# Kernel tuning notes

Measured on AMD Instinct MI355X. Metric: run time of the kernel, lower is better.

The kernel has to match this reference:

```python
import jax, jax.numpy as jnp
import numpy as np

LN_EPS = 1e-12  # config.layer_norm_eps (BERT default)


def setup_inputs() -> dict:
    key = jax.random.key(0)
    k1, k2, k3, k4 = jax.random.split(key, 4)
    B, S, D_IN, D_OUT = 16, 512, 4096, 1024
    return {
        "hidden_states": jax.random.normal(k1, (B, S, D_IN), dtype=jnp.float32),
        "input_tensor": jax.random.normal(k2, (B, S, D_OUT), dtype=jnp.float32),
        "W": jax.random.normal(k3, (D_OUT, D_IN), dtype=jnp.float32) * 0.02,
        "b": jax.random.normal(k4, (D_OUT,), dtype=jnp.float32) * 0.02,
        "gamma": jnp.ones((D_OUT,), dtype=jnp.float32),
        "beta": jnp.zeros((D_OUT,), dtype=jnp.float32),
    }


def reference(hidden_states, input_tensor, W, b, gamma, beta):
    # mix_Linear 1-bit path (XNOR-Net style): binarize weights with per-row scale
    alpha = jnp.mean(jnp.abs(W), axis=1, keepdims=True)   # [D_OUT, 1]
    W_q = jnp.sign(W) * alpha                              # [D_OUT, D_IN]
    # dense GEMM: [B,S,D_IN] x [D_OUT,D_IN]^T -> [B,S,D_OUT]
    h = jnp.einsum("bsi,oi->bso", hidden_states, W_q) + b
    # dropout is identity in eval mode; residual add + LayerNorm
    x = h + input_tensor
    mu = jnp.mean(x, axis=-1, keepdims=True)
    var = jnp.mean(jnp.square(x - mu), axis=-1, keepdims=True)
    return gamma * (x - mu) * jax.lax.rsqrt(var + LN_EPS) + beta
```

## Files before the change

kernel.cpp:

```cpp
#include <hip/hip_runtime.h>
#include <hip/hip_bf16.h>

using u16    = unsigned short;
using short8 = __attribute__((ext_vector_type(8))) short;
using u16x4  = __attribute__((ext_vector_type(4))) u16;
using f32x4  = __attribute__((ext_vector_type(4))) float;

#define M_DIM 8192
#define N_DIM 1024
#define K_DIM 4096

typedef __attribute__((address_space(1))) void gvoid;
typedef __attribute__((address_space(3))) void svoid;
#define GLOAD_LDS16(g, s) \
  __builtin_amdgcn_global_load_lds((gvoid*)(void*)(g), (svoid*)(s), 16, 0, 0)

__global__ __launch_bounds__(256) void wprep_kernel(const float* __restrict__ W,
                                                    u16* __restrict__ Wsgn,
                                                    float* __restrict__ alpha) {
  const int row = blockIdx.x;
  const int t   = threadIdx.x;
  const float4* wr = (const float4*)(W + (size_t)row * K_DIM);
  float4 v[4];
  float s = 0.f;
#pragma unroll
  for (int j = 0; j < 4; ++j) {
    v[j] = wr[t + 256 * j];
    s += fabsf(v[j].x) + fabsf(v[j].y) + fabsf(v[j].z) + fabsf(v[j].w);
  }
#pragma unroll
  for (int off = 32; off > 0; off >>= 1) s += __shfl_down(s, off, 64);
  __shared__ float red[4];
  if ((t & 63) == 0) red[t >> 6] = s;
  __syncthreads();
  if (t == 0) alpha[row] = (red[0] + red[1] + red[2] + red[3]) * (1.0f / K_DIM);
  u16x4* dst = (u16x4*)(Wsgn + (size_t)row * K_DIM);
#pragma unroll
  for (int j = 0; j < 4; ++j) {
    u16x4 sg;
    sg[0] = v[j].x > 0.f ? 0x3F80 : (v[j].x < 0.f ? 0xBF80 : 0);
    sg[1] = v[j].y > 0.f ? 0x3F80 : (v[j].y < 0.f ? 0xBF80 : 0);
    sg[2] = v[j].z > 0.f ? 0x3F80 : (v[j].z < 0.f ? 0xBF80 : 0);
    sg[3] = v[j].w > 0.f ? 0x3F80 : (v[j].w < 0.f ? 0xBF80 : 0);
    dst[t + 256 * j] = sg;
  }
}

__device__ __forceinline__ short8 pack_bf16x8(f32x4 lo, f32x4 hi) {
  union { short8 s; __hip_bfloat162 h[4]; } u;
  u.h[0] = __float22bfloat162_rn(make_float2(lo[0], lo[1]));
  u.h[1] = __float22bfloat162_rn(make_float2(lo[2], lo[3]));
  u.h[2] = __float22bfloat162_rn(make_float2(hi[0], hi[1]));
  u.h[3] = __float22bfloat162_rn(make_float2(hi[2], hi[3]));
  return u.s;
}

__global__ __launch_bounds__(256) void gemm_kernel(const float* __restrict__ A,
                                                   const u16* __restrict__ Bsgn,
                                                   const float* __restrict__ alpha,
                                                   const float* __restrict__ bias,
                                                   const float* __restrict__ resid,
                                                   float* __restrict__ out) {
  __shared__ float lA[2][128 * 32];
  __shared__ u16   lB[128 * 64];
  const int tid  = threadIdx.x;
  const int wave = tid >> 6;
  const int lane = tid & 63;
  const int quad = lane >> 4;
  const int l16  = lane & 15;
  const int wm   = (wave >> 1) * 64;
  const int wn   = (wave & 1) * 64;

  const int b    = blockIdx.x;
  const int xcd  = b & 7;
  const int l    = b >> 3;
  const size_t m0 = (size_t)(xcd * 8 + (l >> 3)) * 128;
  const size_t n0 = (size_t)(l & 7) * 128;

  f32x4 acc[4][4] = {};

  const int r8 = lane >> 3;
  const int s_ = lane & 7;

  const u16*   bsrc[4];
  u16*         bdst[4];
  const float* a0src[4];
  const float* a1src[4];
  float*       a0dst[4];
  float*       a1dst[4];
#pragma unroll
  for (int j = 0; j < 4; ++j) {
    const int c   = wave * 4 + j;
    const int row = c * 8 + r8;
    bsrc[j]  = Bsgn + (n0 + (size_t)row) * K_DIM + (size_t)((s_ ^ r8) * 8);
    bdst[j]  = lB + c * 512;
    a0src[j] = A + (m0 + (size_t)row) * K_DIM + (size_t)((s_ ^ r8) * 8);
    a1src[j] = a0src[j] + 4;
    a0dst[j] = &lA[0][c * 256 + lane * 4];
    a1dst[j] = &lA[1][c * 256 + lane * 4];
  }

  for (int k0 = 0; k0 < K_DIM; k0 += 64) {
#pragma unroll
    for (int j = 0; j < 4; ++j) GLOAD_LDS16(bsrc[j] + k0, bdst[j]);
#pragma unroll
    for (int j = 0; j < 4; ++j) GLOAD_LDS16(a0src[j] + k0, a0dst[j]);
#pragma unroll
    for (int j = 0; j < 4; ++j) GLOAD_LDS16(a1src[j] + k0, a1dst[j]);
    asm volatile("s_waitcnt vmcnt(0)" ::: "memory");
    __syncthreads();

#pragma unroll
    for (int s = 0; s < 2; ++s) {
      const int kq = s * 4 + quad;
      short8 af[4], bf[4];
#pragma unroll
      for (int mt = 0; mt < 4; ++mt) {
        const int row  = wm + mt * 16 + l16;
        const int slot = kq ^ (row & 7);
        f32x4 lo = *(const f32x4*)(&lA[0][row * 32 + slot * 4]);
        f32x4 hi = *(const f32x4*)(&lA[1][row * 32 + slot * 4]);
        af[mt] = pack_bf16x8(lo, hi);
      }
#pragma unroll
      for (int nt = 0; nt < 4; ++nt) {
        const int col = wn + nt * 16 + l16;
        bf[nt] = *(const short8*)(lB + col * 64 + ((kq ^ (col & 7)) * 8));
      }
#pragma unroll
      for (int mt = 0; mt < 4; ++mt)
#pragma unroll
        for (int nt = 0; nt < 4; ++nt)
          acc[mt][nt] = __builtin_amdgcn_mfma_f32_16x16x32_bf16(af[mt], bf[nt],
                                                                acc[mt][nt], 0, 0, 0);
    }
    __syncthreads();
  }

#pragma unroll
  for (int nt = 0; nt < 4; ++nt) {
    const size_t n  = n0 + wn + nt * 16 + l16;
    const float  al = alpha[n];
    const float  bi = bias[n];
#pragma unroll
    for (int mt = 0; mt < 4; ++mt) {
      const size_t mbase = m0 + wm + mt * 16 + quad * 4;
#pragma unroll
      for (int r = 0; r < 4; ++r) {
        const size_t mm = mbase + r;
        out[mm * N_DIM + n] = acc[mt][nt][r] * al + bi + resid[mm * N_DIM + n];
      }
    }
  }
}

__global__ __launch_bounds__(256) void ln_kernel(float* __restrict__ x,
                                                 const float* __restrict__ gamma,
                                                 const float* __restrict__ beta) {
  const size_t row = blockIdx.x;
  float4* xr = (float4*)(x + row * N_DIM);
  const int t = threadIdx.x;
  float4 v = xr[t];
  float s  = v.x + v.y + v.z + v.w;
  float sq = v.x * v.x + v.y * v.y + v.z * v.z + v.w * v.w;
#pragma unroll
  for (int off = 32; off > 0; off >>= 1) {
    s  += __shfl_down(s, off, 64);
    sq += __shfl_down(sq, off, 64);
  }
  __shared__ float rs[4], rq[4];
  if ((t & 63) == 0) { rs[t >> 6] = s; rq[t >> 6] = sq; }
  __syncthreads();
  s  = rs[0] + rs[1] + rs[2] + rs[3];
  sq = rq[0] + rq[1] + rq[2] + rq[3];
  const float mu  = s * (1.0f / N_DIM);
  float var = sq * (1.0f / N_DIM) - mu * mu;
  var = fmaxf(var, 0.0f);
  const float inv = rsqrtf(var + 1e-12f);
  const float4 g = ((const float4*)gamma)[t];
  const float4 b = ((const float4*)beta)[t];
  v.x = g.x * ((v.x - mu) * inv) + b.x;
  v.y = g.y * ((v.y - mu) * inv) + b.y;
  v.z = g.z * ((v.z - mu) * inv) + b.z;
  v.w = g.w * ((v.w - mu) * inv) + b.w;
  xr[t] = v;
}

extern "C" void kernel_launch(void* const* d_in, const int* in_sizes, int n_in,
                              void* d_out, int out_size, void* d_ws, size_t ws_size,
                              hipStream_t stream) {
  const float* hidden = (const float*)d_in[0];
  const float* resid  = (const float*)d_in[1];
  const float* W      = (const float*)d_in[2];
  const float* bias   = (const float*)d_in[3];
  const float* gamma  = (const float*)d_in[4];
  const float* beta   = (const float*)d_in[5];
  float* out = (float*)d_out;

  char* ws = (char*)d_ws;
  u16*   Wsgn  = (u16*)ws;
  float* alpha = (float*)(ws + 8ull * 1024 * 1024);

  wprep_kernel<<<N_DIM, 256, 0, stream>>>(W, Wsgn, alpha);

  const int nblocks = (N_DIM / 128) * (M_DIM / 128);
  gemm_kernel<<<nblocks, 256, 0, stream>>>(hidden, Wsgn, alpha, bias, resid, out);

  ln_kernel<<<M_DIM, 256, 0, stream>>>(out, gamma, beta);
}
```

Before: 360.8 us.

## Double-buffer GEMM LDS and convert A to bf16 in registers before staging

The GEMM main loop becomes double-buffered. The next K tile of the sign-weight matrix is fetched straight into LDS while MFMAs run on the current tile. A is now loaded into registers, converted to bf16 once per element, and written to LDS as bf16. This halves A's LDS footprint, removes the repeated fp32-to-bf16 packing inside the compute loop, and overlaps global loads with math. The cost is more VGPRs for the staged A registers, which could lower occupancy.

```diff
diff --git a/kernel.cpp b/kernel.cpp
--- a/kernel.cpp
+++ b/kernel.cpp
@@ -61,8 +61,8 @@
                                                    const float* __restrict__ bias,
                                                    const float* __restrict__ resid,
                                                    float* __restrict__ out) {
-  __shared__ float lA[2][128 * 32];
-  __shared__ u16   lB[128 * 64];
+  __shared__ u16 lA[2][128 * 64];
+  __shared__ u16 lB[2][128 * 64];
   const int tid  = threadIdx.x;
   const int wave = tid >> 6;
   const int lane = tid & 63;
@@ -81,61 +81,80 @@
 
   const int r8 = lane >> 3;
   const int s_ = lane & 7;
-
-  const u16*   bsrc[4];
-  u16*         bdst[4];
-  const float* a0src[4];
-  const float* a1src[4];
-  float*       a0dst[4];
-  float*       a1dst[4];
+  const u16* bsrc[4];
+  int        bdstoff[4];
 #pragma unroll
   for (int j = 0; j < 4; ++j) {
-    const int c   = wave * 4 + j;
-    const int row = c * 8 + r8;
-    bsrc[j]  = Bsgn + (n0 + (size_t)row) * K_DIM + (size_t)((s_ ^ r8) * 8);
-    bdst[j]  = lB + c * 512;
-    a0src[j] = A + (m0 + (size_t)row) * K_DIM + (size_t)((s_ ^ r8) * 8);
-    a1src[j] = a0src[j] + 4;
-    a0dst[j] = &lA[0][c * 256 + lane * 4];
-    a1dst[j] = &lA[1][c * 256 + lane * 4];
-  }
-
-  for (int k0 = 0; k0 < K_DIM; k0 += 64) {
-#pragma unroll
-    for (int j = 0; j < 4; ++j) GLOAD_LDS16(bsrc[j] + k0, bdst[j]);
-#pragma unroll
-    for (int j = 0; j < 4; ++j) GLOAD_LDS16(a0src[j] + k0, a0dst[j]);
-#pragma unroll
-    for (int j = 0; j < 4; ++j) GLOAD_LDS16(a1src[j] + k0, a1dst[j]);
+    const int c = wave * 4 + j;
+    bsrc[j]    = Bsgn + (n0 + (size_t)(c * 8 + r8)) * K_DIM + (size_t)((s_ ^ r8) * 8);
+    bdstoff[j] = c * 512;
+  }
+
+  const int arow = tid >> 1;
+  const int ah   = tid & 1;
+  const float* asrc = A + (m0 + (size_t)arow) * K_DIM + ah * 32;
+  int awoff[4];
+#pragma unroll
+  for (int g = 0; g < 4; ++g) {
+    const int G = ah * 4 + g;
+    awoff[g] = arow * 64 + ((G ^ (arow & 7)) * 8);
+  }
+
+  f32x4 ar[8];
+
+#define A_ISSUE(K0)                                                        \
+  _Pragma("unroll")                                                        \
+  for (int j = 0; j < 8; ++j) ar[j] = *(const f32x4*)(asrc + (K0) + j * 4);
+
+#define B_ISSUE(K0, BUF)                                                   \
+  _Pragma("unroll")                                                        \
+  for (int j = 0; j < 4; ++j) GLOAD_LDS16(bsrc[j] + (K0), &lB[BUF][bdstoff[j]]);
+
+#define A_WRITE(BUF)                                                       \
+  _Pragma("unroll")                                                        \
+  for (int g = 0; g < 4; ++g)                                              \
+    *(short8*)(&lA[BUF][awoff[g]]) = pack_bf16x8(ar[2 * g], ar[2 * g + 1]);
+
+#define COMPUTE(BUF)                                                       \
+  _Pragma("unroll")                                                        \
+  for (int s = 0; s < 2; ++s) {                                            \
+    const int kq = s * 4 + quad;                                           \
+    short8 af[4], bf[4];                                                   \
+    _Pragma("unroll")                                                      \
+    for (int mt = 0; mt < 4; ++mt) {                                       \
+      const int row = wm + mt * 16 + l16;                                  \
+      af[mt] = *(const short8*)(&lA[BUF][row * 64 + ((kq ^ (row & 7)) * 8)]); \
+    }                                                                      \
+    _Pragma("unroll")                                                      \
+    for (int nt = 0; nt < 4; ++nt) {                                       \
+      const int col = wn + nt * 16 + l16;                                  \
+      bf[nt] = *(const short8*)(&lB[BUF][col * 64 + ((kq ^ (col & 7)) * 8)]); \
+    }                                                                      \
+    _Pragma("unroll")                                                      \
+    for (int mt = 0; mt < 4; ++mt)                                         \
+      _Pragma("unroll")                                                    \
+      for (int nt = 0; nt < 4; ++nt)                                       \
+        acc[mt][nt] = __builtin_amdgcn_mfma_f32_16x16x32_bf16(af[mt], bf[nt], \
+                                                              acc[mt][nt], 0, 0, 0); \
+  }
+
+  A_ISSUE(0);
+  B_ISSUE(0, 0);
+  A_WRITE(0);
+  __syncthreads();
+
+  int cur = 0;
+#pragma unroll 1
+  for (int k0 = 0; k0 < K_DIM - 64; k0 += 64) {
+    A_ISSUE(k0 + 64);
+    B_ISSUE(k0 + 64, cur ^ 1);
+    COMPUTE(cur);
     asm volatile("s_waitcnt vmcnt(0)" ::: "memory");
+    A_WRITE(cur ^ 1);
     __syncthreads();
-
-#pragma unroll
-    for (int s = 0; s < 2; ++s) {
-      const int kq = s * 4 + quad;
-      short8 af[4], bf[4];
-#pragma unroll
-      for (int mt = 0; mt < 4; ++mt) {
-        const int row  = wm + mt * 16 + l16;
-        const int slot = kq ^ (row & 7);
-        f32x4 lo = *(const f32x4*)(&lA[0][row * 32 + slot * 4]);
-        f32x4 hi = *(const f32x4*)(&lA[1][row * 32 + slot * 4]);
-        af[mt] = pack_bf16x8(lo, hi);
-      }
-#pragma unroll
-      for (int nt = 0; nt < 4; ++nt) {
-        const int col = wn + nt * 16 + l16;
-        bf[nt] = *(const short8*)(lB + col * 64 + ((kq ^ (col & 7)) * 8));
-      }
-#pragma unroll
-      for (int mt = 0; mt < 4; ++mt)
-#pragma unroll
-        for (int nt = 0; nt < 4; ++nt)
-          acc[mt][nt] = __builtin_amdgcn_mfma_f32_16x16x32_bf16(af[mt], bf[nt],
-                                                                acc[mt][nt], 0, 0, 0);
-    }
-    __syncthreads();
-  }
+    cur ^= 1;
+  }
+  COMPUTE(cur);
 
 #pragma unroll
   for (int nt = 0; nt < 4; ++nt) {
@@ -152,6 +171,10 @@
       }
     }
   }
+#undef A_ISSUE
+#undef B_ISSUE
+#undef A_WRITE
+#undef COMPUTE
 }
 
 __global__ __launch_bounds__(256) void ln_kernel(float* __restrict__ x,
```

After: 394.7 us. +9.4%, slower.
